# Kernel optimization log

Hardware: AMD Instinct MI355X
Metric: run time of the kernel (lower is better)

## Reference

```python
import jax, jax.numpy as jnp
import numpy as np

B, V, H, L = 256, 50000, 1024, 2

def setup_inputs() -> dict:
    key = jax.random.key(0)
    ks = jax.random.split(key, 9)
    s = 1.0 / np.sqrt(H)
    return {
        "input_ids": jax.random.randint(ks[0], (B,), 0, V),
        "hidden": jax.random.normal(ks[1], (L, B, H), jnp.float32),
        "emb": jax.random.normal(ks[2], (V, H), jnp.float32) * 0.02,
        "w_ih": jax.random.uniform(ks[3], (L, 3 * H, H), jnp.float32, -s, s),
        "w_hh": jax.random.uniform(ks[4], (L, 3 * H, H), jnp.float32, -s, s),
        "b_ih": jax.random.uniform(ks[5], (L, 3 * H), jnp.float32, -s, s),
        "b_hh": jax.random.uniform(ks[6], (L, 3 * H), jnp.float32, -s, s),
        "dec_w": jax.random.uniform(ks[7], (V, H), jnp.float32, -s, s),
        "dec_b": jax.random.uniform(ks[8], (V,), jnp.float32, -s, s),
    }

def _gru_cell(x, h, w_ih_l, w_hh_l, b_ih_l, b_hh_l):
    # PyTorch GRU cell math. x: [B,H], h: [B,H]
    gi = x @ w_ih_l.T + b_ih_l          # [B, 3H]
    gh = h @ w_hh_l.T + b_hh_l          # [B, 3H]
    i_r, i_z, i_n = jnp.split(gi, 3, axis=-1)
    h_r, h_z, h_n = jnp.split(gh, 3, axis=-1)
    r = jax.nn.sigmoid(i_r + h_r)
    z = jax.nn.sigmoid(i_z + h_z)
    n = jnp.tanh(i_n + r * h_n)
    return (1.0 - z) * n + z * h

def reference(input_ids, hidden, emb, w_ih, w_hh, b_ih, b_hh, dec_w, dec_b):
    x = emb[input_ids]                  # embedding gather: [B, H]
    new_h = []
    for l in range(hidden.shape[0]):    # small fixed n_layers loop
        h_new = _gru_cell(x, hidden[l], w_ih[l], w_hh[l], b_ih[l], b_hh[l])
        new_h.append(h_new)
        x = h_new                       # output of layer l feeds layer l+1
    hidden_out = jnp.stack(new_h)       # [L, B, H]
    logits = x @ dec_w.T + dec_b        # [B, V]
    return logits, hidden_out
```

## Files before the change

### kernel.cpp

```cpp
#include <hip/hip_runtime.h>

#define KDIM 1024

typedef __attribute__((ext_vector_type(8))) short bf16x8;
typedef __attribute__((ext_vector_type(4))) short short4v;
typedef __attribute__((ext_vector_type(4))) float f32x4;

__device__ __forceinline__ short f2bf(float f) {
    union { float f; unsigned u; } x; x.f = f;
    unsigned r = x.u + 0x7fffu + ((x.u >> 16) & 1u);
    return (short)(r >> 16);
}

__device__ __forceinline__ bf16x8 cvt8(f32x4 a, f32x4 b) {
    union { unsigned u[4]; bf16x8 v; } r;
    asm("v_cvt_pk_bf16_f32 %0, %1, %2" : "=v"(r.u[0]) : "v"(a.x), "v"(a.y));
    asm("v_cvt_pk_bf16_f32 %0, %1, %2" : "=v"(r.u[1]) : "v"(a.z), "v"(a.w));
    asm("v_cvt_pk_bf16_f32 %0, %1, %2" : "=v"(r.u[2]) : "v"(b.x), "v"(b.y));
    asm("v_cvt_pk_bf16_f32 %0, %1, %2" : "=v"(r.u[3]) : "v"(b.z), "v"(b.w));
    return r.v;
}

__device__ __forceinline__ void gload16(const void* g, void* l) {
    __builtin_amdgcn_global_load_lds(
        (const __attribute__((address_space(1))) void*)g,
        (__attribute__((address_space(3))) void*)l, 16, 0, 0);
}

#define WAIT_VM(n) asm volatile("s_waitcnt vmcnt(" #n ")" ::: "memory")
#define BARRIER() do { asm volatile("" ::: "memory"); \
                       __builtin_amdgcn_s_barrier();  \
                       asm volatile("" ::: "memory"); } while (0)

template<int NF, bool PRED>
__launch_bounds__(256, 2)
__global__ void gemm_pipe(const short* __restrict__ A0, const float* __restrict__ W0,
                          float* __restrict__ C0, int nb0,
                          const short* __restrict__ A1, const float* __restrict__ W1,
                          float* __restrict__ C1,
                          const float* __restrict__ bias, int N, int ldc)
{
    constexpr int WBYTES = NF * 4096;
    constexpr int BUFB   = 16384 + WBYTES;
    __shared__ __align__(1024) char lds[3 * BUFB];

    const int bx = blockIdx.x;
    const short* A; const float* W; float* C; int n0;
    if (bx < nb0) { A = A0; W = W0; C = C0; n0 = bx * (32 * NF); }
    else          { A = A1; W = W1; C = C1; n0 = (bx - nb0) * (32 * NF); }

    const int t = threadIdx.x;
    const int lane = t & 63;
    const int w = t >> 6;
    const int wr = w >> 1;
    const int wc = w & 1;

    const float* gW[NF];
    #pragma unroll
    for (int i = 0; i < NF; ++i) {
        int sl = (i * 4 + w) * 64 + lane;
        int row = sl >> 3, cc = sl & 7;
        int rowg = n0 + row;
        if (PRED) rowg = (rowg < N) ? rowg : (N - 1);
        gW[i] = W + (size_t)rowg * KDIM + ((cc ^ (row & 7)) << 2);
    }
    const short* gA[4];
    #pragma unroll
    for (int j = 0; j < 4; ++j)
        gA[j] = A + (size_t)(j * 4 + w) * 16384 + lane * 8;

    f32x4 acc[8][NF];
    #pragma unroll
    for (int i = 0; i < 8; ++i)
        #pragma unroll
        for (int j = 0; j < NF; ++j)
            acc[i][j] = (f32x4){0.f, 0.f, 0.f, 0.f};

    auto stage = [&](int s, int buf) {
        char* base = lds + buf * BUFB;
        #pragma unroll
        for (int i = 0; i < NF; ++i)
            gload16(gW[i] + s * 32, base + 16384 + (i * 4 + w) * 1024);
        #pragma unroll
        for (int j = 0; j < 4; ++j)
            gload16(gA[j] + s * 512, base + (j * 4 + w) * 1024);
    };

    auto compute = [&](int buf) {
        const char* base = lds + buf * BUFB;
        const char* Wb = base + 16384;
        bf16x8 bfr[NF];
        #pragma unroll
        for (int nf = 0; nf < NF; ++nf) {
            int row = (wc * NF + nf) * 16 + (lane & 15);
            int c0 = (lane >> 4) << 1;
            f32x4 lo = *(const f32x4*)(Wb + row * 128 + ((c0 ^ (row & 7)) << 4));
            f32x4 hi = *(const f32x4*)(Wb + row * 128 + (((c0 + 1) ^ (row & 7)) << 4));
            bfr[nf] = cvt8(lo, hi);
        }
        #pragma unroll
        for (int mf = 0; mf < 8; ++mf) {
            bf16x8 a = *(const bf16x8*)(base + (wr * 8 + mf) * 1024 + lane * 16);
            #pragma unroll
            for (int nf = 0; nf < NF; ++nf)
                acc[mf][nf] = __builtin_amdgcn_mfma_f32_16x16x32_bf16(a, bfr[nf], acc[mf][nf], 0, 0, 0);
        }
    };

    stage(0, 0);
    stage(1, 1);

    int bc = 0, bp = 2;
    for (int s = 0; s < 32; ++s) {
        if (s + 2 < 32) {
            stage(s + 2, bp);
            if constexpr (NF == 2) WAIT_VM(12); else WAIT_VM(10);
        } else if (s + 2 == 32) {
            if constexpr (NF == 2) WAIT_VM(6); else WAIT_VM(5);
        } else {
            WAIT_VM(0);
        }
        BARRIER();
        compute(bc);
        BARRIER();
        bc = (bc == 2) ? 0 : bc + 1;
        bp = (bp == 2) ? 0 : bp + 1;
    }

    #pragma unroll
    for (int mf = 0; mf < 8; ++mf) {
        int row = wr * 128 + mf * 16 + ((lane >> 4) << 2);
        #pragma unroll
        for (int nf = 0; nf < NF; ++nf) {
            int col = n0 + (wc * NF + nf) * 16 + (lane & 15);
            if (PRED && col >= N) continue;
            float bv = bias ? bias[col] : 0.0f;
            #pragma unroll
            for (int r = 0; r < 4; ++r)
                C[(size_t)(row + r) * ldc + col] = acc[mf][nf][r] + bv;
        }
    }
}

__global__ void prep_kernel(const int* __restrict__ ids, const float* __restrict__ hidden,
                            const float* __restrict__ emb,
                            short* __restrict__ x_frag, short* __restrict__ h_frag)
{
    const int m = blockIdx.x;
    const int which = blockIdx.y;
    const int j = threadIdx.x << 3;

    const float* src;
    short* dst;
    if (which == 0) { src = emb + (size_t)ids[m] * KDIM; dst = x_frag; }
    else {
        src = hidden + ((size_t)(which - 1) * 256 + m) * KDIM;
        dst = h_frag + (size_t)(which - 1) * 256 * KDIM;
    }
    f32x4 v0 = *(const f32x4*)(src + j);
    f32x4 v1 = *(const f32x4*)(src + j + 4);
    int mf = m >> 4, rr = m & 15, kf = j >> 5, g = (j >> 3) & 3;
    short* p = dst + (size_t)((mf * 32 + kf) * 64 + g * 16 + rr) * 8;
    short4v a, b;
    a.x = f2bf(v0.x); a.y = f2bf(v0.y); a.z = f2bf(v0.z); a.w = f2bf(v0.w);
    b.x = f2bf(v1.x); b.y = f2bf(v1.y); b.z = f2bf(v1.z); b.w = f2bf(v1.w);
    *(short4v*)p = a;
    *(short4v*)(p + 4) = b;
}

__global__ void gate_kernel(const float* __restrict__ gi, const float* __restrict__ gh,
                            const float* __restrict__ bi, const float* __restrict__ bh,
                            const float* __restrict__ hprev, float* __restrict__ hout,
                            short* __restrict__ x_frag)
{
    const int m = blockIdx.x;
    const int j = threadIdx.x << 3;
    const float* gim = gi + (size_t)m * 3072;
    const float* ghm = gh + (size_t)m * 3072;
    const float* hp = hprev + (size_t)m * KDIM;
    float* ho = hout + (size_t)m * KDIM;
    int mf = m >> 4, rr = m & 15, kf = j >> 5, g = (j >> 3) & 3;
    short* xp = x_frag + (size_t)((mf * 32 + kf) * 64 + g * 16 + rr) * 8;

    #pragma unroll
    for (int half = 0; half < 2; ++half) {
        int jj = j + half * 4;
        f32x4 vir = *(const f32x4*)(gim + jj);
        f32x4 viz = *(const f32x4*)(gim + 1024 + jj);
        f32x4 vin = *(const f32x4*)(gim + 2048 + jj);
        f32x4 vhr = *(const f32x4*)(ghm + jj);
        f32x4 vhz = *(const f32x4*)(ghm + 1024 + jj);
        f32x4 vhn = *(const f32x4*)(ghm + 2048 + jj);
        f32x4 bir = *(const f32x4*)(bi + jj);
        f32x4 biz = *(const f32x4*)(bi + 1024 + jj);
        f32x4 bin = *(const f32x4*)(bi + 2048 + jj);
        f32x4 bhr = *(const f32x4*)(bh + jj);
        f32x4 bhz = *(const f32x4*)(bh + 1024 + jj);
        f32x4 bhn = *(const f32x4*)(bh + 2048 + jj);
        f32x4 vh  = *(const f32x4*)(hp + jj);
        f32x4 outv;
        short4v xb;
        #pragma unroll
        for (int e = 0; e < 4; ++e) {
            float r = 1.f / (1.f + __expf(-(vir[e] + bir[e] + vhr[e] + bhr[e])));
            float z = 1.f / (1.f + __expf(-(viz[e] + biz[e] + vhz[e] + bhz[e])));
            float n = tanhf(vin[e] + bin[e] + r * (vhn[e] + bhn[e]));
            outv[e] = (1.f - z) * n + z * vh[e];
        }
        *(f32x4*)(ho + jj) = outv;
        xb.x = f2bf(outv[0]); xb.y = f2bf(outv[1]); xb.z = f2bf(outv[2]); xb.w = f2bf(outv[3]);
        *(short4v*)(xp + half * 4) = xb;
    }
}

extern "C" void kernel_launch(void* const* d_in, const int* in_sizes, int n_in,
                              void* d_out, int out_size, void* d_ws, size_t ws_size,
                              hipStream_t stream)
{
    const int*   ids    = (const int*)d_in[0];
    const float* hidden = (const float*)d_in[1];
    const float* emb    = (const float*)d_in[2];
    const float* w_ih   = (const float*)d_in[3];
    const float* w_hh   = (const float*)d_in[4];
    const float* b_ih   = (const float*)d_in[5];
    const float* b_hh   = (const float*)d_in[6];
    const float* dec_w  = (const float*)d_in[7];
    const float* dec_b  = (const float*)d_in[8];

    float* out = (float*)d_out;
    float* logits = out;
    float* hidden_out = out + (size_t)256 * 50000;

    short* x_frag = (short*)d_ws;
    short* h_frag = x_frag + 256 * 1024;
    float* gi = logits;
    float* gh = logits + (size_t)256 * 3072;

    prep_kernel<<<dim3(256, 3), 128, 0, stream>>>(ids, hidden, emb, x_frag, h_frag);

    for (int l = 0; l < 2; ++l) {
        gemm_pipe<1, false><<<192, 256, 0, stream>>>(
            x_frag, w_ih + (size_t)l * 3072 * 1024, gi, 96,
            h_frag + (size_t)l * 256 * 1024, w_hh + (size_t)l * 3072 * 1024, gh,
            nullptr, 3072, 3072);
        gate_kernel<<<256, 128, 0, stream>>>(
            gi, gh, b_ih + (size_t)l * 3072, b_hh + (size_t)l * 3072,
            hidden + (size_t)l * 256 * 1024,
            hidden_out + (size_t)l * 256 * 1024, x_frag);
    }

    gemm_pipe<2, true><<<782, 256, 0, stream>>>(
        x_frag, dec_w, logits, 782,
        x_frag, dec_w, logits,
        dec_b, 50000, 50000);
}
```

Measured before the change: 128.7 us.

## Add dedicated decoder GEMM kernel with register-staged double-buffered weight tiles

Replaces the generic pipelined GEMM for the vocab decoder with a new kernel. Each 512-thread block owns a 128-column tile across all 256 rows. Activations (pre-swizzled bf16 fragments) are read straight from global memory. Weights are loaded as fp32 through registers, converted to bf16, and written into a swizzled, double-buffered LDS tile, with the next K quarter's loads interleaved with the current MFMAs. This halves the block count and removes the global-to-LDS async pipeline. The risks are register pressure from the 64 KB LDS buffers and repeated uncached global reads of the A fragments.

```diff
diff --git a/kernel.cpp b/kernel.cpp
--- a/kernel.cpp
+++ b/kernel.cpp
@@ -5,6 +5,7 @@
 typedef __attribute__((ext_vector_type(8))) short bf16x8;
 typedef __attribute__((ext_vector_type(4))) short short4v;
 typedef __attribute__((ext_vector_type(4))) float f32x4;
+typedef __attribute__((ext_vector_type(2))) unsigned uint2v;
 
 __device__ __forceinline__ short f2bf(float f) {
     union { float f; unsigned u; } x; x.f = f;
@@ -27,10 +28,121 @@
         (__attribute__((address_space(3))) void*)l, 16, 0, 0);
 }
 
-#define WAIT_VM(n) asm volatile("s_waitcnt vmcnt(" #n ")" ::: "memory")
+#define WAIT_VM(n)  asm volatile("s_waitcnt vmcnt(" #n ")" ::: "memory")
+#define BARSYNC() do { asm volatile("s_waitcnt lgkmcnt(0)" ::: "memory"); \
+                       __builtin_amdgcn_s_barrier();                      \
+                       asm volatile("" ::: "memory"); } while (0)
 #define BARRIER() do { asm volatile("" ::: "memory"); \
                        __builtin_amdgcn_s_barrier();  \
                        asm volatile("" ::: "memory"); } while (0)
+
+__launch_bounds__(512, 2)
+__global__ void gemm_dec4(const short* __restrict__ A, const float* __restrict__ W,
+                          float* __restrict__ C, const float* __restrict__ bias, int N)
+{
+    __shared__ __align__(1024) char lds[2][65536];
+
+    const int n0 = blockIdx.x * 128;
+    const int t = threadIdx.x;
+    const int lane = t & 63;
+    const int w = t >> 6;
+    const int wr = w >> 1;
+    const int wcq = w & 1;
+    const int cl = lane & 15;
+    const int kc = lane >> 4;
+
+    auto wload = [&](int kq, int j) -> f32x4 {
+        int rowg = n0 + w * 16 + j;
+        rowg = (rowg < N) ? rowg : (N - 1);
+        return *(const f32x4*)(W + (size_t)rowg * KDIM + kq * 256 + lane * 4);
+    };
+    auto wstore = [&](int buf, int j, f32x4 v) {
+        const int rowL = w * 16 + j;
+        unsigned lo, hi;
+        asm("v_cvt_pk_bf16_f32 %0, %1, %2" : "=v"(lo) : "v"(v.x), "v"(v.y));
+        asm("v_cvt_pk_bf16_f32 %0, %1, %2" : "=v"(hi) : "v"(v.z), "v"(v.w));
+        int addr = rowL * 512 + ((((lane >> 1) ^ (rowL & 7))) << 4) + ((lane & 1) << 3);
+        uint2v d; d.x = lo; d.y = hi;
+        *(uint2v*)(lds[buf] + addr) = d;
+    };
+
+    float bv[4];
+    #pragma unroll
+    for (int nf = 0; nf < 4; ++nf) {
+        int col = n0 + wcq * 64 + nf * 16 + cl;
+        bv[nf] = bias[col < N ? col : 0];
+    }
+
+    f32x4 acc[4][4];
+    #pragma unroll
+    for (int i = 0; i < 4; ++i)
+        #pragma unroll
+        for (int j = 0; j < 4; ++j)
+            acc[i][j] = (f32x4){0.f, 0.f, 0.f, 0.f};
+
+    #pragma unroll
+    for (int h = 0; h < 2; ++h) {
+        f32x4 tmp[8];
+        #pragma unroll
+        for (int j = 0; j < 8; ++j) tmp[j] = wload(0, h * 8 + j);
+        #pragma unroll
+        for (int j = 0; j < 8; ++j) wstore(0, h * 8 + j, tmp[j]);
+    }
+    BARSYNC();
+
+    #pragma unroll
+    for (int kq = 0; kq < 4; ++kq) {
+        const int buf = kq & 1;
+        const char* Bb = lds[buf];
+        f32x4 ring[8];
+        if (kq < 3) {
+            #pragma unroll
+            for (int j = 0; j < 8; ++j) ring[j] = wload(kq + 1, j);
+        }
+        #pragma unroll
+        for (int kf = 0; kf < 8; ++kf) {
+            if (kq < 3) {
+                wstore(buf ^ 1, 2 * kf,     ring[(2 * kf)     & 7]);
+                wstore(buf ^ 1, 2 * kf + 1, ring[(2 * kf + 1) & 7]);
+                if (kf < 4) {
+                    ring[(2 * kf)     & 7] = wload(kq + 1, 2 * kf + 8);
+                    ring[(2 * kf + 1) & 7] = wload(kq + 1, 2 * kf + 9);
+                }
+            }
+            const int kfg = kq * 8 + kf;
+            bf16x8 a[4], b[4];
+            #pragma unroll
+            for (int mf = 0; mf < 4; ++mf)
+                a[mf] = *(const bf16x8*)(A + (size_t)(((wr * 4 + mf) * 32 + kfg) * 64 + lane) * 8);
+            #pragma unroll
+            for (int nf = 0; nf < 4; ++nf) {
+                int row = wcq * 64 + nf * 16 + cl;
+                int c = kf * 4 + kc;
+                b[nf] = *(const bf16x8*)(Bb + row * 512 + ((c ^ (row & 7)) << 4));
+            }
+            #pragma unroll
+            for (int mf = 0; mf < 4; ++mf)
+                #pragma unroll
+                for (int nf = 0; nf < 4; ++nf)
+                    acc[mf][nf] = __builtin_amdgcn_mfma_f32_16x16x32_bf16(a[mf], b[nf], acc[mf][nf], 0, 0, 0);
+        }
+        BARSYNC();
+    }
+
+    #pragma unroll
+    for (int mf = 0; mf < 4; ++mf) {
+        int row = wr * 64 + mf * 16 + kc * 4;
+        #pragma unroll
+        for (int nf = 0; nf < 4; ++nf) {
+            int col = n0 + wcq * 64 + nf * 16 + cl;
+            if (col < N) {
+                #pragma unroll
+                for (int r = 0; r < 4; ++r)
+                    C[(size_t)(row + r) * N + col] = acc[mf][nf][r] + bv[nf];
+            }
+        }
+    }
+}
 
 template<int NF, bool PRED>
 __launch_bounds__(256, 2)
@@ -134,10 +246,10 @@
         for (int nf = 0; nf < NF; ++nf) {
             int col = n0 + (wc * NF + nf) * 16 + (lane & 15);
             if (PRED && col >= N) continue;
-            float bv = bias ? bias[col] : 0.0f;
+            float bvv = bias ? bias[col] : 0.0f;
             #pragma unroll
             for (int r = 0; r < 4; ++r)
-                C[(size_t)(row + r) * ldc + col] = acc[mf][nf][r] + bv;
+                C[(size_t)(row + r) * ldc + col] = acc[mf][nf][r] + bvv;
         }
     }
 }
@@ -249,8 +361,5 @@
             hidden_out + (size_t)l * 256 * 1024, x_frag);
     }
 
-    gemm_pipe<2, true><<<782, 256, 0, stream>>>(
-        x_frag, dec_w, logits, 782,
-        x_frag, dec_w, logits,
-        dec_b, 50000, 50000);
-}
+    gemm_dec4<<<392, 512, 0, stream>>>(x_frag, dec_w, logits, dec_b, 50000);
+}
```

Measured after the change: 139.1 us. 8.0% more time.

## Add warp-specialized decoder GEMM with producer/consumer waves and register-staged weight streaming

Applied to the files above, without the earlier changes.

Replaces the decoder projection GEMM with a new 512-thread kernel in which four waves stream fp32 weight rows into swizzled bf16 LDS tiles while the other four waves run MFMA on the previous tile. The A operand (the activation fragments) is read straight from global memory instead of being staged through LDS. The goal is to overlap the memory-bound weight stream with compute and to cut LDS traffic. In exchange, half the waves do no MFMA, occupancy is one block per CU because of the 128KB LDS, and each block pipelines only two 32-row phases.

```diff
diff --git a/kernel.cpp b/kernel.cpp
--- a/kernel.cpp
+++ b/kernel.cpp
@@ -5,6 +5,7 @@
 typedef __attribute__((ext_vector_type(8))) short bf16x8;
 typedef __attribute__((ext_vector_type(4))) short short4v;
 typedef __attribute__((ext_vector_type(4))) float f32x4;
+typedef __attribute__((ext_vector_type(2))) unsigned uint2v;
 
 __device__ __forceinline__ short f2bf(float f) {
     union { float f; unsigned u; } x; x.f = f;
@@ -27,10 +28,119 @@
         (__attribute__((address_space(3))) void*)l, 16, 0, 0);
 }
 
-#define WAIT_VM(n) asm volatile("s_waitcnt vmcnt(" #n ")" ::: "memory")
+#define WAIT_VM(n)  asm volatile("s_waitcnt vmcnt(" #n ")" ::: "memory")
+#define BARSYNC() do { asm volatile("s_waitcnt lgkmcnt(0)" ::: "memory"); \
+                       __builtin_amdgcn_s_barrier();                      \
+                       asm volatile("" ::: "memory"); } while (0)
 #define BARRIER() do { asm volatile("" ::: "memory"); \
                        __builtin_amdgcn_s_barrier();  \
                        asm volatile("" ::: "memory"); } while (0)
+
+__launch_bounds__(512, 1)
+__global__ void gemm_dec5(const short* __restrict__ A, const float* __restrict__ W,
+                          float* __restrict__ C, const float* __restrict__ bias, int N)
+{
+    __shared__ __align__(1024) char lds[2][65536];
+
+    const int n0 = blockIdx.x * 64;
+    const int t = threadIdx.x;
+    const int lane = t & 63;
+    const int w = t >> 6;
+    const int cl = lane & 15;
+    const int kc = lane >> 4;
+
+    auto wstore = [&](char* base, int r, int q, f32x4 v) {
+        unsigned lo, hi;
+        asm("v_cvt_pk_bf16_f32 %0, %1, %2" : "=v"(lo) : "v"(v.x), "v"(v.y));
+        asm("v_cvt_pk_bf16_f32 %0, %1, %2" : "=v"(hi) : "v"(v.z), "v"(v.w));
+        int c = q * 32 + (lane >> 1);
+        int addr = r * 2048 + (((c ^ (r & 7))) << 4) + ((lane & 1) << 3);
+        uint2v d; d.x = lo; d.y = hi;
+        *(uint2v*)(base + addr) = d;
+    };
+
+    auto stream_rows = [&](int ph, int buf, int r0, int nr) {
+        char* base = lds[buf];
+        int rowg = n0 + ph * 32 + r0;
+        rowg = rowg < N ? rowg : N - 1;
+        const float* src = W + (size_t)rowg * KDIM + lane * 4;
+        f32x4 c0 = *(const f32x4*)(src);
+        f32x4 c1 = *(const f32x4*)(src + 256);
+        f32x4 c2 = *(const f32x4*)(src + 512);
+        f32x4 c3 = *(const f32x4*)(src + 768);
+        for (int r = r0; r < r0 + nr; ++r) {
+            f32x4 d0, d1, d2, d3;
+            if (r + 1 < r0 + nr) {
+                int rg = n0 + ph * 32 + r + 1;
+                rg = rg < N ? rg : N - 1;
+                const float* s2 = W + (size_t)rg * KDIM + lane * 4;
+                d0 = *(const f32x4*)(s2);
+                d1 = *(const f32x4*)(s2 + 256);
+                d2 = *(const f32x4*)(s2 + 512);
+                d3 = *(const f32x4*)(s2 + 768);
+            }
+            wstore(base, r, 0, c0);
+            wstore(base, r, 1, c1);
+            wstore(base, r, 2, c2);
+            wstore(base, r, 3, c3);
+            c0 = d0; c1 = d1; c2 = d2; c3 = d3;
+        }
+    };
+
+    auto consume = [&](int ph, int buf) {
+        const char* base = lds[buf];
+        const int cw = w - 4;
+        f32x4 acc[4][2];
+        #pragma unroll
+        for (int i = 0; i < 4; ++i) {
+            acc[i][0] = (f32x4){0.f, 0.f, 0.f, 0.f};
+            acc[i][1] = (f32x4){0.f, 0.f, 0.f, 0.f};
+        }
+        #pragma unroll
+        for (int kf = 0; kf < 32; ++kf) {
+            bf16x8 a[4], b[2];
+            #pragma unroll
+            for (int mf = 0; mf < 4; ++mf)
+                a[mf] = *(const bf16x8*)(A + (size_t)(((cw * 4 + mf) * 32 + kf) * 64 + lane) * 8);
+            #pragma unroll
+            for (int nf = 0; nf < 2; ++nf) {
+                int row = nf * 16 + cl;
+                b[nf] = *(const bf16x8*)(base + row * 2048 + (((kf * 4 + kc) ^ (row & 7)) << 4));
+            }
+            #pragma unroll
+            for (int mf = 0; mf < 4; ++mf) {
+                acc[mf][0] = __builtin_amdgcn_mfma_f32_16x16x32_bf16(a[mf], b[0], acc[mf][0], 0, 0, 0);
+                acc[mf][1] = __builtin_amdgcn_mfma_f32_16x16x32_bf16(a[mf], b[1], acc[mf][1], 0, 0, 0);
+            }
+        }
+        #pragma unroll
+        for (int mf = 0; mf < 4; ++mf) {
+            int row = cw * 64 + mf * 16 + kc * 4;
+            #pragma unroll
+            for (int nf = 0; nf < 2; ++nf) {
+                int col = n0 + ph * 32 + nf * 16 + cl;
+                if (col < N) {
+                    float bv = bias[col];
+                    #pragma unroll
+                    for (int r = 0; r < 4; ++r)
+                        C[(size_t)(row + r) * N + col] = acc[mf][nf][r] + bv;
+                }
+            }
+        }
+    };
+
+    stream_rows(0, 0, w * 4, 4);
+    BARSYNC();
+
+    if (w < 4) {
+        stream_rows(1, 1, w * 8, 8);
+    } else {
+        consume(0, 0);
+    }
+    BARSYNC();
+
+    if (w >= 4) consume(1, 1);
+}
 
 template<int NF, bool PRED>
 __launch_bounds__(256, 2)
@@ -134,10 +244,10 @@
         for (int nf = 0; nf < NF; ++nf) {
             int col = n0 + (wc * NF + nf) * 16 + (lane & 15);
             if (PRED && col >= N) continue;
-            float bv = bias ? bias[col] : 0.0f;
+            float bvv = bias ? bias[col] : 0.0f;
             #pragma unroll
             for (int r = 0; r < 4; ++r)
-                C[(size_t)(row + r) * ldc + col] = acc[mf][nf][r] + bv;
+                C[(size_t)(row + r) * ldc + col] = acc[mf][nf][r] + bvv;
         }
     }
 }
@@ -249,8 +359,5 @@
             hidden_out + (size_t)l * 256 * 1024, x_frag);
     }
 
-    gemm_pipe<2, true><<<782, 256, 0, stream>>>(
-        x_frag, dec_w, logits, 782,
-        x_frag, dec_w, logits,
-        dec_b, 50000, 50000);
-}
+    gemm_dec5<<<782, 512, 0, stream>>>(x_frag, dec_w, logits, dec_b, 50000);
+}
```

Result: slower. 184.0 us (+43.0%).
